# Optimization experiments

Measured on AMD Instinct MI355X. Metric: run time of the kernel, lower is better.

## Reference

```python
import jax, jax.numpy as jnp
import numpy as np

GROUPS = 32
EPS = 1e-5


def _group_norm(x, w, b):
    B, C, H, W = x.shape
    xr = x.reshape(B, GROUPS, C // GROUPS, H, W)
    mean = xr.mean(axis=(2, 3, 4), keepdims=True)
    var = xr.var(axis=(2, 3, 4), keepdims=True)
    xn = ((xr - mean) * jax.lax.rsqrt(var + EPS)).reshape(B, C, H, W)
    return xn * w[None, :, None, None] + b[None, :, None, None]


def _conv1x1(w, b, x):
    # 1x1 conv == per-pixel channel matmul
    return jnp.einsum('oc,bchw->bohw', w, x) + b[None, :, None, None]


def setup_inputs() -> dict:
    key = jax.random.key(0)
    ks = jax.random.split(key, 6)
    C = 512
    s = 1.0 / np.sqrt(C)  # kaiming-uniform-ish scale for 1x1 convs
    return {
        'x': jax.random.normal(ks[0], (4, C, 64, 64), jnp.float32),
        'gn_w': jnp.ones((C,), jnp.float32),
        'gn_b': jnp.zeros((C,), jnp.float32),
        'qw': jax.random.normal(ks[1], (C, C), jnp.float32) * s,
        'qb': jnp.zeros((C,), jnp.float32),
        'kw': jax.random.normal(ks[2], (C, C), jnp.float32) * s,
        'kb': jnp.zeros((C,), jnp.float32),
        'vw': jax.random.normal(ks[3], (C, C), jnp.float32) * s,
        'vb': jnp.zeros((C,), jnp.float32),
        'pw': jax.random.normal(ks[4], (C, C), jnp.float32) * s,
        'pb': jnp.zeros((C,), jnp.float32),
    }


def reference(x, gn_w, gn_b, qw, qb, kw, kb, vw, vb, pw, pb):
    B, C, H, W = x.shape
    h_ = _group_norm(x, gn_w, gn_b)
    q = _conv1x1(qw, qb, h_).reshape(B, C, H * W)
    k = _conv1x1(kw, kb, h_).reshape(B, C, H * W)
    v = _conv1x1(vw, vb, h_).reshape(B, C, H * W)
    # scores [B, HW(query), HW(key)]
    scores = jnp.einsum('bcq,bck->bqk', q, k) * (C ** -0.5)
    attn = jax.nn.softmax(scores, axis=-1)
    out = jnp.einsum('bqk,bdk->bdq', attn, v).reshape(B, C, H, W)
    return x + _conv1x1(pw, pb, out)
```

## Files before the change

### kernel.cpp

```cpp
#include <hip/hip_runtime.h>

#define DEV __device__ __forceinline__

typedef __attribute__((ext_vector_type(8))) short short8;
typedef __attribute__((ext_vector_type(4))) float floatx4;
typedef __attribute__((ext_vector_type(16))) float floatx16;
typedef __attribute__((ext_vector_type(4))) int i32x4;
typedef __attribute__((ext_vector_type(8))) int i32x8;
typedef __attribute__((ext_vector_type(2))) long longx2;

DEV unsigned short f2bs(float x) {
    unsigned u = __float_as_uint(x);
    unsigned r = (u + 0x7fffu + ((u >> 16) & 1u)) >> 16;
    return (unsigned short)r;
}

DEV unsigned char f2fp8(float x) {
#if __has_builtin(__builtin_amdgcn_cvt_pk_fp8_f32)
    int pk = __builtin_amdgcn_cvt_pk_fp8_f32(x, 0.f, 0, false);
    return (unsigned char)(pk & 0xff);
#else
    unsigned u = __float_as_uint(x);
    unsigned s = (u >> 24) & 0x80;
    unsigned a = u & 0x7fffffff;
    unsigned um = a + 0x7ffffu + ((a >> 20) & 1u);
    unsigned r = (a >= 0x3c800000u) ? ((um >> 20) - 0x3C0u) : 0u;
    return (unsigned char)(r | s);
#endif
}

DEV unsigned pack_fp8x4(float v0, float v1, float v2, float v3) {
#if __has_builtin(__builtin_amdgcn_cvt_pk_fp8_f32)
    unsigned pk = (unsigned)__builtin_amdgcn_cvt_pk_fp8_f32(v0, v1, 0, false);
    pk = (unsigned)__builtin_amdgcn_cvt_pk_fp8_f32(v2, v3, (int)pk, true);
    return pk;
#else
    return (unsigned)f2fp8(v0) | ((unsigned)f2fp8(v1) << 8) |
           ((unsigned)f2fp8(v2) << 16) | ((unsigned)f2fp8(v3) << 24);
#endif
}

DEV unsigned pack_i8x4(float v0, float v1, float v2, float v3) {
    unsigned b0 = (unsigned)((int)rintf(v0)) & 255u;
    unsigned b1 = (unsigned)((int)rintf(v1)) & 255u;
    unsigned b2 = (unsigned)((int)rintf(v2)) & 255u;
    unsigned b3 = (unsigned)((int)rintf(v3)) & 255u;
    return b0 | (b1 << 8) | (b2 << 16) | (b3 << 24);
}

DEV void syncfull() {
    asm volatile("s_waitcnt vmcnt(0) lgkmcnt(0)" ::: "memory");
    __builtin_amdgcn_sched_barrier(0);
    __builtin_amdgcn_s_barrier();
    __builtin_amdgcn_sched_barrier(0);
}

__global__ void pre_kernel(const float* __restrict__ x,
                           const float* __restrict__ qw, const float* __restrict__ kw,
                           const float* __restrict__ vw, const float* __restrict__ pw,
                           const float* __restrict__ qb, const float* __restrict__ kb,
                           unsigned short* __restrict__ wqkb, unsigned short* __restrict__ wvb,
                           unsigned short* __restrict__ wpb,
                           float* __restrict__ biasqk,
                           float* __restrict__ stats) {
    int b = blockIdx.x, tid = threadIdx.x;
    if (b < 768) {
        const float* src = (b < 256) ? qw : (b < 512) ? kw : vw;
        unsigned short* dst = (b < 256) ? wqkb : (b < 512) ? (wqkb + 262144) : wvb;
        int off = (b & 255) * 256 + tid;
        float4 v = ((const float4*)src)[off];
        ushort4 o;
        o.x = f2bs(v.x); o.y = f2bs(v.y); o.z = f2bs(v.z); o.w = f2bs(v.w);
        ((ushort4*)dst)[off] = o;
    } else if (b < 1024) {
        int off = (b - 768) * 256 + tid;
        int row = off >> 7, c4 = (off & 127) * 4;
        float4 v = ((const float4*)pw)[off];
        float vv[4] = {v.x, v.y, v.z, v.w};
#pragma unroll
        for (int e = 0; e < 4; ++e) {
            int c = c4 + e;
            int cp = (c & ~63) | (((c & 31) << 1) | ((c >> 5) & 1));
            wpb[row * 512 + cp] = f2bs(vv[e]);
        }
    } else if (b == 1024) {
        biasqk[tid]       = qb[tid];
        biasqk[256 + tid] = qb[256 + tid];
        biasqk[512 + tid] = kb[tid];
        biasqk[768 + tid] = kb[256 + tid];
    } else {
        int bg = b - 1025;
        const float4* p = (const float4*)(x + (size_t)bg * 65536);
        float s = 0.f, ss = 0.f;
        for (int i = tid; i < 16384; i += 256) {
            float4 v = p[i];
            s += v.x + v.y + v.z + v.w;
            ss += v.x * v.x + v.y * v.y + v.z * v.z + v.w * v.w;
        }
        for (int off = 32; off; off >>= 1) { s += __shfl_down(s, off); ss += __shfl_down(ss, off); }
        __shared__ float rs[4], rss[4];
        int wave = tid >> 6, lane = tid & 63;
        if (lane == 0) { rs[wave] = s; rss[wave] = ss; }
        __syncthreads();
        if (tid == 0) {
            float S = rs[0] + rs[1] + rs[2] + rs[3];
            float SS = rss[0] + rss[1] + rss[2] + rss[3];
            float mean = S * (1.f / 65536.f);
            float var = SS * (1.f / 65536.f) - mean * mean;
            stats[bg * 2] = mean;
            stats[bg * 2 + 1] = rsqrtf(var + 1e-5f);
        }
    }
}

__global__ void gn_apply_kernel(const float* __restrict__ x, const float* __restrict__ stats,
                                const float* __restrict__ gw, const float* __restrict__ gb,
                                unsigned short* __restrict__ ht) {
    __shared__ __align__(16) unsigned short t[64][72];
    int b = blockIdx.z, c0 = blockIdx.y * 64, p0 = blockIdx.x * 64;
    int tid = threadIdx.x;
    const float* xb = x + ((size_t)b * 512 + c0) * 4096 + p0;
#pragma unroll
    for (int pass = 0; pass < 4; ++pass) {
        int cl = pass * 16 + (tid >> 4);
        int pq = (tid & 15) * 4;
        float4 v = *(const float4*)(xb + (size_t)cl * 4096 + pq);
        int c = c0 + cl, g = c >> 4;
        float mean = stats[(b * 32 + g) * 2], rstd = stats[(b * 32 + g) * 2 + 1];
        float sw = gw[c] * rstd;
        float sb = gb[c] - mean * sw;
        t[pq + 0][cl] = f2bs(v.x * sw + sb);
        t[pq + 1][cl] = f2bs(v.y * sw + sb);
        t[pq + 2][cl] = f2bs(v.z * sw + sb);
        t[pq + 3][cl] = f2bs(v.w * sw + sb);
    }
    __syncthreads();
    unsigned short* hb = ht + ((size_t)b * 4096 + p0) * 512 + c0;
#pragma unroll
    for (int pass = 0; pass < 2; ++pass) {
        int pl = pass * 32 + (tid >> 3);
        int c8 = (tid & 7) * 8;
        *(uint4*)(hb + (size_t)pl * 512 + c8) = *(const uint4*)&t[pl][c8];
    }
}

__global__ void gemm_qkv(const unsigned short* __restrict__ h_t, long long sP,
                         const unsigned short* __restrict__ wqkb,
                         const unsigned short* __restrict__ wvb,
                         char* __restrict__ q_i8, char* __restrict__ k_i8,
                         char* __restrict__ v_f8,
                         const float* __restrict__ biasqk, const float* __restrict__ vb,
                         float qs) {
    __shared__ __align__(16) unsigned short lA[128 * 64];
    __shared__ __align__(16) unsigned short lB[128 * 64];
    const int tid = threadIdx.x;
    const int wave = tid >> 6, lane = tid & 63;
    const int flat = blockIdx.x;
    const bool isqk = flat < 1024;
    int m0, n0, bz;
    const unsigned short *Ab, *Bb;
    if (isqk) {
        m0 = ((flat >> 3) & 31) * 128;
        n0 = (flat & 7) * 128;
        bz = flat >> 8;
        Ab = h_t + (size_t)bz * sP;
        Bb = wqkb;
    } else {
        const int g = flat - 1024;
        m0 = ((g >> 5) & 3) * 128;
        n0 = (g & 31) * 128;
        bz = g >> 7;
        Ab = wvb;
        Bb = h_t + (size_t)bz * sP;
    }

    floatx4 acc[4][4];
#pragma unroll
    for (int i = 0; i < 4; i++)
#pragma unroll
        for (int j = 0; j < 4; j++) acc[i][j] = (floatx4){0.f, 0.f, 0.f, 0.f};

    const int wm = (wave >> 1) * 64, wn = (wave & 1) * 64;
    const int quad = lane >> 4;
    const int lc = lane & 15;
    const int lc7 = lc & 7;

    for (int kt = 0; kt < 8; ++kt) {
        const int kbase = kt * 64;
#pragma unroll
        for (int c = 0; c < 4; ++c) {
            int d = c * 256 + tid;
            int r = d >> 3;
            int kc = (d & 7) ^ (r & 7);
            const unsigned short* ga = Ab + (size_t)(m0 + r) * 512 + kbase + kc * 8;
            const unsigned short* gb = Bb + (size_t)(n0 + r) * 512 + kbase + kc * 8;
            __builtin_amdgcn_global_load_lds(
                (const __attribute__((address_space(1))) void*)ga,
                (__attribute__((address_space(3))) void*)&lA[(size_t)(c * 256 + wave * 64) * 8], 16, 0, 0);
            __builtin_amdgcn_global_load_lds(
                (const __attribute__((address_space(1))) void*)gb,
                (__attribute__((address_space(3))) void*)&lB[(size_t)(c * 256 + wave * 64) * 8], 16, 0, 0);
        }
        __syncthreads();
#pragma unroll
        for (int kk = 0; kk < 2; ++kk) {
            const int swz = ((kk * 4 + quad) ^ lc7) * 8;
            short8 af[4], bf[4];
#pragma unroll
            for (int i = 0; i < 4; i++)
                af[i] = *(const short8*)&lA[(size_t)(wm + i * 16 + lc) * 64 + swz];
#pragma unroll
            for (int j = 0; j < 4; j++)
                bf[j] = *(const short8*)&lB[(size_t)(wn + j * 16 + lc) * 64 + swz];
#pragma unroll
            for (int i = 0; i < 4; i++)
#pragma unroll
                for (int j = 0; j < 4; j++)
                    acc[i][j] = __builtin_amdgcn_mfma_f32_16x16x32_bf16(af[i], bf[j], acc[i][j], 0, 0, 0);
        }
        __syncthreads();
    }

    const int rowb = quad * 4;
    if (isqk) {
#pragma unroll
        for (int i = 0; i < 4; i++) {
#pragma unroll
            for (int r = 0; r < 4; r++) {
                const int m = m0 + wm + i * 16 + rowb + r;
                float q[4];
#pragma unroll
                for (int j = 0; j < 4; j++) {
                    const int n = n0 + wn + j * 16 + lc;
                    q[j] = fminf(fmaxf((acc[i][j][r] + biasqk[n]) * qs, -127.f), 127.f);
                }
                const int col64 = n0 + wn;
                char* outp = (col64 < 512) ? q_i8 : k_i8;
                size_t idx = (size_t)bz * sP + (size_t)m * 512 +
                             (col64 - ((col64 < 512) ? 0 : 512)) + lc * 4;
                *(unsigned*)(outp + idx) = pack_i8x4(q[0], q[1], q[2], q[3]);
            }
        }
    } else {
#pragma unroll
        for (int i = 0; i < 4; i++) {
#pragma unroll
            for (int r = 0; r < 4; r++) {
                const int m = m0 + wm + i * 16 + rowb + r;
                const float bm = vb[m];
                float q[4];
#pragma unroll
                for (int j = 0; j < 4; j++)
                    q[j] = fminf(fmaxf(acc[i][j][r] + bm, -448.f), 448.f);
                size_t idx = (size_t)bz * sP + (size_t)m * 4096 + n0 + wn + lc * 4;
                *(unsigned*)(v_f8 + idx) = pack_fp8x4(q[0], q[1], q[2], q[3]);
            }
        }
    }
}

__global__ void gemm_proj(const unsigned short* __restrict__ A,
                          const unsigned short* __restrict__ B, long long sBb,
                          float* __restrict__ Cv, long long sCb,
                          const float* __restrict__ bias,
                          const float* __restrict__ resid, long long sRb,
                          const float* __restrict__ rsum,
                          int M, int N, int K) {
    __shared__ __align__(16) unsigned short lA[128 * 64];
    __shared__ __align__(16) unsigned short lB[128 * 64];
    const int tid = threadIdx.x;
    const int wave = tid >> 6, lane = tid & 63;
    const int m0 = blockIdx.y * 128, n0 = blockIdx.x * 128, bz = blockIdx.z;
    const unsigned short* Ab = A;
    const unsigned short* Bb = B + (size_t)bz * sBb;

    floatx4 acc[4][4];
#pragma unroll
    for (int i = 0; i < 4; i++)
#pragma unroll
        for (int j = 0; j < 4; j++) acc[i][j] = (floatx4){0.f, 0.f, 0.f, 0.f};

    const int wm = (wave >> 1) * 64, wn = (wave & 1) * 64;
    const int quad = lane >> 4;
    const int lc = lane & 15;
    const int lc7 = lc & 7;

    const int nk = K >> 6;
    for (int kt = 0; kt < nk; ++kt) {
        const int kbase = kt * 64;
#pragma unroll
        for (int c = 0; c < 4; ++c) {
            int d = c * 256 + tid;
            int r = d >> 3;
            int kc = (d & 7) ^ (r & 7);
            const unsigned short* ga = Ab + (size_t)(m0 + r) * 512 + ((kbase & 511) + kc * 8);
            const unsigned short* gb = Bb + (size_t)(n0 + r) * 1024 + kbase + kc * 8;
            __builtin_amdgcn_global_load_lds(
                (const __attribute__((address_space(1))) void*)ga,
                (__attribute__((address_space(3))) void*)&lA[(size_t)(c * 256 + wave * 64) * 8], 16, 0, 0);
            __builtin_amdgcn_global_load_lds(
                (const __attribute__((address_space(1))) void*)gb,
                (__attribute__((address_space(3))) void*)&lB[(size_t)(c * 256 + wave * 64) * 8], 16, 0, 0);
        }
        __syncthreads();
#pragma unroll
        for (int kk = 0; kk < 2; ++kk) {
            const int swz = ((kk * 4 + quad) ^ lc7) * 8;
            short8 af[4], bf[4];
#pragma unroll
            for (int i = 0; i < 4; i++)
                af[i] = *(const short8*)&lA[(size_t)(wm + i * 16 + lc) * 64 + swz];
#pragma unroll
            for (int j = 0; j < 4; j++)
                bf[j] = *(const short8*)&lB[(size_t)(wn + j * 16 + lc) * 64 + swz];
#pragma unroll
            for (int i = 0; i < 4; i++)
#pragma unroll
                for (int j = 0; j < 4; j++)
                    acc[i][j] = __builtin_amdgcn_mfma_f32_16x16x32_bf16(af[i], bf[j], acc[i][j], 0, 0, 0);
        }
        __syncthreads();
    }

    float rsinv[4];
#pragma unroll
    for (int j = 0; j < 4; j++) {
        const int n = n0 + wn + j * 16 + lc;
        rsinv[j] = 1.f / (rsum[(size_t)bz * 4096 + n] + rsum[(size_t)(4 + bz) * 4096 + n]);
    }

    const int rowb = quad * 4;
#pragma unroll
    for (int i = 0; i < 4; i++) {
#pragma unroll
        for (int r = 0; r < 4; r++) {
            const int m = m0 + wm + i * 16 + rowb + r;
            const float bm = bias[m];
#pragma unroll
            for (int j = 0; j < 4; j++) {
                const int n = n0 + wn + j * 16 + lc;
                size_t idx = (size_t)bz * sCb + (size_t)m * N + n;
                Cv[idx] = acc[i][j][r] * rsinv[j] + bm + resid[(size_t)bz * sRb + (size_t)m * N + n];
            }
        }
    }
}

__global__ __launch_bounds__(512, 2) void attn_fused(
    const char* __restrict__ Qg, const char* __restrict__ Kg,
    const char* __restrict__ Vg,
    unsigned short* __restrict__ Ou, long long sOb,
    float* __restrict__ rsum, float scale2) {
    __shared__ __align__(16) char Ql[512 * 128];
    __shared__ __align__(16) char Kl[256 * 128];
    __shared__ __align__(16) char Vl[256 * 128];
    __shared__ __align__(16) char Pl[64 * 128];
    const int tid = threadIdx.x;
    const int wave = tid >> 6, lane = tid & 63;
    const int quad = lane >> 4, lc = lane & 15;
    const int lc7 = lc & 7;
    const int l31 = lane & 31, lh = lane >> 5;
    const int id = blockIdx.x;
    const int xcd = id & 7, qi = id >> 3;
    const int bz = xcd >> 1, split = xcd & 1;
    const int q0 = qi * 128;
    const int kvbase = split * 2048;
    const int NIT = 32;

    const char* Qb = Qg + ((size_t)bz * 4096 + q0) * 512;
    const char* Kb = Kg + ((size_t)bz * 4096 + kvbase) * 512;
    const char* Vb = Vg + (size_t)bz * 2097152 + kvbase;

    const int wq = wave * 16;
    const int mO = (wave >> 2) * 64, nO = (wave & 3) * 128;

    auto stageQ = [&]() {
#pragma unroll
        for (int c = 0; c < 8; ++c) {
            int f = c * 512 + tid;
            int rr = f >> 3, cs = f & 7;
            int qq = rr & 127, chq = rr >> 7;
            int s = cs ^ (qq & 7);
            __builtin_amdgcn_global_load_lds(
                (const __attribute__((address_space(1))) void*)(Qb + (size_t)qq * 512 + chq * 128 + s * 16),
                (__attribute__((address_space(3))) void*)(Ql + (size_t)f * 16), 16, 0, 0);
        }
    };
    auto stageK = [&](int t) {
#pragma unroll
        for (int c = 0; c < 4; ++c) {
            int f = c * 512 + tid;
            int rr = f >> 3, cs = f & 7;
            int kv = rr & 63, chq = rr >> 6;
            int s = cs ^ (kv & 7);
            __builtin_amdgcn_global_load_lds(
                (const __attribute__((address_space(1))) void*)(Kb + (size_t)(t * 64 + kv) * 512 + chq * 128 + s * 16),
                (__attribute__((address_space(3))) void*)(Kl + (size_t)f * 16), 16, 0, 0);
        }
    };
    auto stageV = [&](int t) {
#pragma unroll
        for (int c = 0; c < 4; ++c) {
            int f = c * 512 + tid;
            int u = (f & 7) ^ ((f >> 3) & 7);
            int d = ((f >> 3) << 1) | (u >> 2);
            int gq = u & 3;
            __builtin_amdgcn_global_load_lds(
                (const __attribute__((address_space(1))) void*)(Vb + (size_t)d * 4096 + t * 64 + gq * 16),
                (__attribute__((address_space(3))) void*)(Vl + (size_t)f * 16), 16, 0, 0);
        }
    };

    floatx16 acco[2][4];
#pragma unroll
    for (int i = 0; i < 2; ++i)
#pragma unroll
        for (int j = 0; j < 4; ++j)
#pragma unroll
            for (int r = 0; r < 16; ++r) acco[i][j][r] = 0.f;
    float rs = 0.f;

    stageQ();
    stageK(0);
    stageV(0);
    syncfull();

    const int q = wq + lc;
    const int q7 = q & 7;

    for (int t = 0; t < NIT; ++t) {
        if (t > 0) stageV(t);
        i32x4 accs[4];
#pragma unroll
        for (int ki = 0; ki < 4; ++ki) accs[ki] = (i32x4){0, 0, 0, 0};
#pragma unroll
        for (int ks = 0; ks < 8; ++ks) {
            const int g = ks * 4 + quad;
            const int gh = g >> 3, gl = g & 7;
            i32x4 bfrag = *(const i32x4*)&Ql[(size_t)(gh * 128 + q) * 128 + ((gl ^ q7) << 4)];
#pragma unroll
            for (int ki = 0; ki < 4; ++ki) {
                const int ar = ki * 16 + lc;
                i32x4 afrag = *(const i32x4*)&Kl[(size_t)(gh * 64 + ar) * 128 + ((gl ^ lc7) << 4)];
                accs[ki] = __builtin_amdgcn_mfma_i32_16x16x64_i8(afrag, bfrag, accs[ki], 0, 0, 0);
            }
        }
        float e[4][4];
#pragma unroll
        for (int ki = 0; ki < 4; ++ki)
#pragma unroll
            for (int r = 0; r < 4; ++r) {
                e[ki][r] = fminf(exp2f(fmaf((float)accs[ki][r], scale2, -2.0f)), 448.f);
                rs += e[ki][r];
            }
        {
            unsigned w0 = pack_fp8x4(e[0][0], e[1][0], e[2][0], e[3][0]);
            unsigned w1 = pack_fp8x4(e[0][1], e[1][1], e[2][1], e[3][1]);
            unsigned w2 = pack_fp8x4(e[0][2], e[1][2], e[2][2], e[3][2]);
            unsigned w3 = pack_fp8x4(e[0][3], e[1][3], e[2][3], e[3][3]);
            const int L = q >> 1;
            const int sl = ((((q & 1) << 2) | quad) ^ (L & 7));
            *(i32x4*)&Pl[(size_t)L * 128 + (sl << 4)] = (i32x4){(int)w0, (int)w1, (int)w2, (int)w3};
        }
        syncfull();

        if (t + 1 < NIT) stageK(t + 1);
        {
            i32x8 pa[2], vv[4];
#pragma unroll
            for (int i = 0; i < 2; ++i) {
                const int r_ = mO + i * 32 + l31;
                const int L = r_ >> 1;
                const int sb = ((r_ & 1) << 2) | (lh << 1);
                i32x4 lo = *(const i32x4*)&Pl[(size_t)L * 128 + ((sb ^ (L & 7)) << 4)];
                i32x4 hi = *(const i32x4*)&Pl[(size_t)L * 128 + (((sb | 1) ^ (L & 7)) << 4)];
                pa[i] = __builtin_shufflevector(lo, hi, 0, 1, 2, 3, 4, 5, 6, 7);
            }
#pragma unroll
            for (int j = 0; j < 4; ++j) {
                const int r_ = nO + j * 32 + l31;
                const int L = r_ >> 1;
                const int sb = ((r_ & 1) << 2) | (lh << 1);
                i32x4 lo = *(const i32x4*)&Vl[(size_t)L * 128 + ((sb ^ (L & 7)) << 4)];
                i32x4 hi = *(const i32x4*)&Vl[(size_t)L * 128 + (((sb | 1) ^ (L & 7)) << 4)];
                vv[j] = __builtin_shufflevector(lo, hi, 0, 1, 2, 3, 4, 5, 6, 7);
            }
#pragma unroll
            for (int i = 0; i < 2; ++i)
#pragma unroll
                for (int j = 0; j < 4; ++j)
                    acco[i][j] = __builtin_amdgcn_mfma_scale_f32_32x32x64_f8f6f4(
                        pa[i], vv[j], acco[i][j], 0, 0,
                        0, 0x7f7f7f7f, 0, 0x7f7f7f7f);
        }
        syncfull();
    }

    rs += __shfl_xor(rs, 16);
    rs += __shfl_xor(rs, 32);
    if (quad == 0) rsum[((size_t)(split * 4 + bz)) * 4096 + q0 + q] = rs;

#pragma unroll
    for (int i = 0; i < 2; ++i) {
#pragma unroll
        for (int reg = 0; reg < 16; ++reg) {
            const int m = q0 + mO + i * 32 + (reg & 3) + 8 * (reg >> 2) + 4 * lh;
            unsigned u01 = (unsigned)f2bs(acco[i][0][reg]) | ((unsigned)f2bs(acco[i][1][reg]) << 16);
            unsigned u23 = (unsigned)f2bs(acco[i][2][reg]) | ((unsigned)f2bs(acco[i][3][reg]) << 16);
            unsigned short* base = Ou + (size_t)bz * sOb + (size_t)m * 1024 + split * 512 + nO;
            *(unsigned*)(base + l31 * 2) = u01;
            *(unsigned*)(base + 64 + l31 * 2) = u23;
        }
    }
}

extern "C" void kernel_launch(void* const* d_in, const int* in_sizes, int n_in,
                              void* d_out, int out_size, void* d_ws, size_t ws_size,
                              hipStream_t stream) {
    (void)in_sizes; (void)n_in; (void)out_size; (void)ws_size;
    const float* x   = (const float*)d_in[0];
    const float* gnw = (const float*)d_in[1];
    const float* gnb = (const float*)d_in[2];
    const float* qw  = (const float*)d_in[3];
    const float* qb  = (const float*)d_in[4];
    const float* kw  = (const float*)d_in[5];
    const float* kb  = (const float*)d_in[6];
    const float* vw  = (const float*)d_in[7];
    const float* vb  = (const float*)d_in[8];
    const float* pw  = (const float*)d_in[9];
    const float* pb  = (const float*)d_in[10];
    float* out = (float*)d_out;

    char* ws = (char*)d_ws;
    unsigned short* h_t = (unsigned short*)(ws);
    char* q_i8 = (char*)(ws + (16ull << 20));
    char* k_i8 = (char*)(ws + (32ull << 20));
    char* v_f8 = (char*)(ws + (48ull << 20));
    unsigned short* wqkb = (unsigned short*)(ws + (64ull << 20));
    unsigned short* wvb = (unsigned short*)(ws + (65ull << 20));
    unsigned short* wpb = wvb + 262144;
    float* stats  = (float*)(ws + (66ull << 20));
    float* biasqk = (float*)(ws + (66ull << 20) + 8192);
    float* rowsum = (float*)(ws + (66ull << 20) + 65536);
    unsigned short* o_un = (unsigned short*)(ws + (72ull << 20));

    const long long sP  = 2097152;
    const long long sOb = 4194304;
    const float QS = 16.f;
    const float SC = 0.044194173824159216f / (QS * QS);
    const float LOG2E = 1.4426950408889634f;

    pre_kernel<<<1153, 256, 0, stream>>>(x, qw, kw, vw, pw, qb, kb, wqkb, wvb, wpb,
                                         biasqk, stats);
    gn_apply_kernel<<<dim3(64, 8, 4), 256, 0, stream>>>(x, stats, gnw, gnb, h_t);
    gemm_qkv<<<1536, 256, 0, stream>>>(h_t, sP, wqkb, wvb, q_i8, k_i8, v_f8, biasqk, vb, QS);
    attn_fused<<<dim3(256), 512, 0, stream>>>(q_i8, k_i8, v_f8, o_un, sOb, rowsum,
                                              SC * LOG2E);
    gemm_proj<<<dim3(32, 4, 4), 256, 0, stream>>>(wpb, o_un, sOb, out, sP, pb, x, sP,
                                                  rowsum, 512, 4096, 1024);
}
```

Baseline: 278.8 us.

## Restructure attention kernel: Q in registers, double-buffered K, direct V loads

```diff
diff --git a/kernel.cpp b/kernel.cpp
--- a/kernel.cpp
+++ b/kernel.cpp
@@ -4,10 +4,8 @@
 
 typedef __attribute__((ext_vector_type(8))) short short8;
 typedef __attribute__((ext_vector_type(4))) float floatx4;
-typedef __attribute__((ext_vector_type(16))) float floatx16;
 typedef __attribute__((ext_vector_type(4))) int i32x4;
 typedef __attribute__((ext_vector_type(8))) int i32x8;
-typedef __attribute__((ext_vector_type(2))) long longx2;
 
 DEV unsigned short f2bs(float x) {
     unsigned u = __float_as_uint(x);
@@ -80,7 +78,7 @@
 #pragma unroll
         for (int e = 0; e < 4; ++e) {
             int c = c4 + e;
-            int cp = (c & ~63) | (((c & 31) << 1) | ((c >> 5) & 1));
+            int cp = ((c & 15) << 5) | (c >> 4);
             wpb[row * 512 + cp] = f2bs(vv[e]);
         }
     } else if (b == 1024) {
@@ -351,42 +349,31 @@
     const char* __restrict__ Vg,
     unsigned short* __restrict__ Ou, long long sOb,
     float* __restrict__ rsum, float scale2) {
-    __shared__ __align__(16) char Ql[512 * 128];
-    __shared__ __align__(16) char Kl[256 * 128];
-    __shared__ __align__(16) char Vl[256 * 128];
-    __shared__ __align__(16) char Pl[64 * 128];
+    __shared__ __align__(16) char Kl[2][256 * 128];
     const int tid = threadIdx.x;
     const int wave = tid >> 6, lane = tid & 63;
     const int quad = lane >> 4, lc = lane & 15;
-    const int lc7 = lc & 7;
-    const int l31 = lane & 31, lh = lane >> 5;
     const int id = blockIdx.x;
     const int xcd = id & 7, qi = id >> 3;
     const int bz = xcd >> 1, split = xcd & 1;
     const int q0 = qi * 128;
     const int kvbase = split * 2048;
-    const int NIT = 32;
-
-    const char* Qb = Qg + ((size_t)bz * 4096 + q0) * 512;
+
     const char* Kb = Kg + ((size_t)bz * 4096 + kvbase) * 512;
     const char* Vb = Vg + (size_t)bz * 2097152 + kvbase;
 
     const int wq = wave * 16;
-    const int mO = (wave >> 2) * 64, nO = (wave & 3) * 128;
-
-    auto stageQ = [&]() {
-#pragma unroll
-        for (int c = 0; c < 8; ++c) {
-            int f = c * 512 + tid;
-            int rr = f >> 3, cs = f & 7;
-            int qq = rr & 127, chq = rr >> 7;
-            int s = cs ^ (qq & 7);
-            __builtin_amdgcn_global_load_lds(
-                (const __attribute__((address_space(1))) void*)(Qb + (size_t)qq * 512 + chq * 128 + s * 16),
-                (__attribute__((address_space(3))) void*)(Ql + (size_t)f * 16), 16, 0, 0);
-        }
-    };
-    auto stageK = [&](int t) {
+    const int q = wq + lc;
+
+    i32x4 qreg[8];
+    {
+        const char* Qrow = Qg + ((size_t)bz * 4096 + q0 + q) * 512 + quad * 16;
+#pragma unroll
+        for (int ks = 0; ks < 8; ++ks)
+            qreg[ks] = *(const i32x4*)(Qrow + ks * 64);
+    }
+
+    auto stageK = [&](char* dst, int t) {
 #pragma unroll
         for (int c = 0; c < 4; ++c) {
             int f = c * 512 + tid;
@@ -395,56 +382,27 @@
             int s = cs ^ (kv & 7);
             __builtin_amdgcn_global_load_lds(
                 (const __attribute__((address_space(1))) void*)(Kb + (size_t)(t * 64 + kv) * 512 + chq * 128 + s * 16),
-                (__attribute__((address_space(3))) void*)(Kl + (size_t)f * 16), 16, 0, 0);
+                (__attribute__((address_space(3))) void*)(dst + (size_t)f * 16), 16, 0, 0);
         }
     };
-    auto stageV = [&](int t) {
-#pragma unroll
-        for (int c = 0; c < 4; ++c) {
-            int f = c * 512 + tid;
-            int u = (f & 7) ^ ((f >> 3) & 7);
-            int d = ((f >> 3) << 1) | (u >> 2);
-            int gq = u & 3;
-            __builtin_amdgcn_global_load_lds(
-                (const __attribute__((address_space(1))) void*)(Vb + (size_t)d * 4096 + t * 64 + gq * 16),
-                (__attribute__((address_space(3))) void*)(Vl + (size_t)f * 16), 16, 0, 0);
-        }
-    };
-
-    floatx16 acco[2][4];
-#pragma unroll
-    for (int i = 0; i < 2; ++i)
-#pragma unroll
-        for (int j = 0; j < 4; ++j)
-#pragma unroll
-            for (int r = 0; r < 16; ++r) acco[i][j][r] = 0.f;
+
     float rs = 0.f;
-
-    stageQ();
-    stageK(0);
-    stageV(0);
-    syncfull();
-
-    const int q = wq + lc;
-    const int q7 = q & 7;
-
-    for (int t = 0; t < NIT; ++t) {
-        if (t > 0) stageV(t);
+    auto qk_tile = [&](const char* KL, unsigned* w) {
         i32x4 accs[4];
 #pragma unroll
         for (int ki = 0; ki < 4; ++ki) accs[ki] = (i32x4){0, 0, 0, 0};
+        __builtin_amdgcn_s_setprio(1);
 #pragma unroll
         for (int ks = 0; ks < 8; ++ks) {
-            const int g = ks * 4 + quad;
-            const int gh = g >> 3, gl = g & 7;
-            i32x4 bfrag = *(const i32x4*)&Ql[(size_t)(gh * 128 + q) * 128 + ((gl ^ q7) << 4)];
+            const int g = ks * 4 + quad, gh = g >> 3, gl = g & 7;
 #pragma unroll
             for (int ki = 0; ki < 4; ++ki) {
                 const int ar = ki * 16 + lc;
-                i32x4 afrag = *(const i32x4*)&Kl[(size_t)(gh * 64 + ar) * 128 + ((gl ^ lc7) << 4)];
-                accs[ki] = __builtin_amdgcn_mfma_i32_16x16x64_i8(afrag, bfrag, accs[ki], 0, 0, 0);
+                i32x4 afrag = *(const i32x4*)&KL[(size_t)(gh * 64 + ar) * 128 + ((gl ^ (ar & 7)) << 4)];
+                accs[ki] = __builtin_amdgcn_mfma_i32_16x16x64_i8(afrag, qreg[ks], accs[ki], 0, 0, 0);
             }
         }
+        __builtin_amdgcn_s_setprio(0);
         float e[4][4];
 #pragma unroll
         for (int ki = 0; ki < 4; ++ki)
@@ -453,47 +411,40 @@
                 e[ki][r] = fminf(exp2f(fmaf((float)accs[ki][r], scale2, -2.0f)), 448.f);
                 rs += e[ki][r];
             }
-        {
-            unsigned w0 = pack_fp8x4(e[0][0], e[1][0], e[2][0], e[3][0]);
-            unsigned w1 = pack_fp8x4(e[0][1], e[1][1], e[2][1], e[3][1]);
-            unsigned w2 = pack_fp8x4(e[0][2], e[1][2], e[2][2], e[3][2]);
-            unsigned w3 = pack_fp8x4(e[0][3], e[1][3], e[2][3], e[3][3]);
-            const int L = q >> 1;
-            const int sl = ((((q & 1) << 2) | quad) ^ (L & 7));
-            *(i32x4*)&Pl[(size_t)L * 128 + (sl << 4)] = (i32x4){(int)w0, (int)w1, (int)w2, (int)w3};
-        }
+#pragma unroll
+        for (int r = 0; r < 4; ++r)
+            w[r] = pack_fp8x4(e[0][r], e[1][r], e[2][r], e[3][r]);
+    };
+
+    floatx4 acc[32];
+#pragma unroll
+    for (int j = 0; j < 32; ++j) acc[j] = (floatx4){0.f, 0.f, 0.f, 0.f};
+
+    stageK(Kl[0], 0);
+    stageK(Kl[1], 1);
+    syncfull();
+
+    for (int T = 0; T < 16; ++T) {
+        unsigned wE[4], wO[4];
+        qk_tile(Kl[0], wE);
         syncfull();
-
-        if (t + 1 < NIT) stageK(t + 1);
-        {
-            i32x8 pa[2], vv[4];
-#pragma unroll
-            for (int i = 0; i < 2; ++i) {
-                const int r_ = mO + i * 32 + l31;
-                const int L = r_ >> 1;
-                const int sb = ((r_ & 1) << 2) | (lh << 1);
-                i32x4 lo = *(const i32x4*)&Pl[(size_t)L * 128 + ((sb ^ (L & 7)) << 4)];
-                i32x4 hi = *(const i32x4*)&Pl[(size_t)L * 128 + (((sb | 1) ^ (L & 7)) << 4)];
-                pa[i] = __builtin_shufflevector(lo, hi, 0, 1, 2, 3, 4, 5, 6, 7);
-            }
-#pragma unroll
-            for (int j = 0; j < 4; ++j) {
-                const int r_ = nO + j * 32 + l31;
-                const int L = r_ >> 1;
-                const int sb = ((r_ & 1) << 2) | (lh << 1);
-                i32x4 lo = *(const i32x4*)&Vl[(size_t)L * 128 + ((sb ^ (L & 7)) << 4)];
-                i32x4 hi = *(const i32x4*)&Vl[(size_t)L * 128 + (((sb | 1) ^ (L & 7)) << 4)];
-                vv[j] = __builtin_shufflevector(lo, hi, 0, 1, 2, 3, 4, 5, 6, 7);
-            }
-#pragma unroll
-            for (int i = 0; i < 2; ++i)
-#pragma unroll
-                for (int j = 0; j < 4; ++j)
-                    acco[i][j] = __builtin_amdgcn_mfma_scale_f32_32x32x64_f8f6f4(
-                        pa[i], vv[j], acco[i][j], 0, 0,
-                        0, 0x7f7f7f7f, 0, 0x7f7f7f7f);
+        if (T < 15) stageK(Kl[0], 2 * T + 2);
+        qk_tile(Kl[1], wO);
+        i32x8 aa = (i32x8){(int)wE[0], (int)wE[1], (int)wE[2], (int)wE[3],
+                           (int)wO[0], (int)wO[1], (int)wO[2], (int)wO[3]};
+        const char* Vt = Vb + (size_t)(2 * T) * 64 + quad * 16;
+#pragma unroll
+        for (int j = 0; j < 32; ++j) {
+            const int d = j * 16 + lc;
+            const char* vrow = Vt + (size_t)d * 4096;
+            i32x4 vE = *(const i32x4*)(vrow);
+            i32x4 vO = *(const i32x4*)(vrow + 64);
+            i32x8 bb = __builtin_shufflevector(vE, vO, 0, 1, 2, 3, 4, 5, 6, 7);
+            acc[j] = __builtin_amdgcn_mfma_scale_f32_16x16x128_f8f6f4(
+                aa, bb, acc[j], 0, 0, 0, 0x7f7f7f7f, 0, 0x7f7f7f7f);
         }
         syncfull();
+        if (T < 15) stageK(Kl[1], 2 * T + 3);
     }
 
     rs += __shfl_xor(rs, 16);
@@ -501,15 +452,17 @@
     if (quad == 0) rsum[((size_t)(split * 4 + bz)) * 4096 + q0 + q] = rs;
 
 #pragma unroll
-    for (int i = 0; i < 2; ++i) {
-#pragma unroll
-        for (int reg = 0; reg < 16; ++reg) {
-            const int m = q0 + mO + i * 32 + (reg & 3) + 8 * (reg >> 2) + 4 * lh;
-            unsigned u01 = (unsigned)f2bs(acco[i][0][reg]) | ((unsigned)f2bs(acco[i][1][reg]) << 16);
-            unsigned u23 = (unsigned)f2bs(acco[i][2][reg]) | ((unsigned)f2bs(acco[i][3][reg]) << 16);
-            unsigned short* base = Ou + (size_t)bz * sOb + (size_t)m * 1024 + split * 512 + nO;
-            *(unsigned*)(base + l31 * 2) = u01;
-            *(unsigned*)(base + 64 + l31 * 2) = u23;
+    for (int r = 0; r < 4; ++r) {
+        const int m = q0 + wq + quad * 4 + r;
+        unsigned short* base = Ou + (size_t)bz * sOb + (size_t)m * 1024 + split * 512 + lc * 32;
+#pragma unroll
+        for (int jj = 0; jj < 4; ++jj) {
+            uint4 u;
+            u.x = (unsigned)f2bs(acc[jj * 8 + 0][r]) | ((unsigned)f2bs(acc[jj * 8 + 1][r]) << 16);
+            u.y = (unsigned)f2bs(acc[jj * 8 + 2][r]) | ((unsigned)f2bs(acc[jj * 8 + 3][r]) << 16);
+            u.z = (unsigned)f2bs(acc[jj * 8 + 4][r]) | ((unsigned)f2bs(acc[jj * 8 + 5][r]) << 16);
+            u.w = (unsigned)f2bs(acc[jj * 8 + 6][r]) | ((unsigned)f2bs(acc[jj * 8 + 7][r]) << 16);
+            *(uint4*)(base + jj * 8) = u;
         }
     }
 }
```

After: 934.9 us. 235% more time.
